# Kernel optimization log

Measured on AMD Instinct MI355X. Metric: run time of the kernel, lower is better.

The kernel has to match this reference:

```python
import jax, jax.numpy as jnp
import numpy as np

N_NODES = 100000
N_DIH = 1000000
SCALAR_DIM = 128
HIDDEN = 64
ATTR_DIM = 3


def setup_inputs() -> dict:
    key = jax.random.key(0)
    ks = jax.random.split(key, 10)
    x = jax.random.normal(ks[0], (N_NODES, SCALAR_DIM), dtype=jnp.float32)
    quadra_index = jax.random.randint(ks[1], (4, N_DIH), 0, N_NODES, dtype=jnp.int32)
    quadra_attr = jax.random.normal(ks[2], (N_DIH, ATTR_DIM), dtype=jnp.float32)
    d_in = SCALAR_DIM * 2 + ATTR_DIM
    W1 = jax.random.normal(ks[3], (d_in, HIDDEN), dtype=jnp.float32) / np.sqrt(d_in)
    b1 = jnp.zeros((HIDDEN,), dtype=jnp.float32)
    W2 = jax.random.normal(ks[4], (HIDDEN, HIDDEN), dtype=jnp.float32) / np.sqrt(HIDDEN)
    b2 = jnp.zeros((HIDDEN,), dtype=jnp.float32)
    W3 = jax.random.normal(ks[5], (HIDDEN, SCALAR_DIM), dtype=jnp.float32) / np.sqrt(HIDDEN)
    b3 = jnp.zeros((SCALAR_DIM,), dtype=jnp.float32)
    # o3.Linear on pure scalars ('128x0e'->'128x0e') is a bias-free linear map
    Wout = jax.random.normal(ks[6], (SCALAR_DIM, SCALAR_DIM), dtype=jnp.float32) / np.sqrt(SCALAR_DIM)
    return {"x": x, "quadra_index": quadra_index, "quadra_attr": quadra_attr,
            "W1": W1, "b1": b1, "W2": W2, "b2": b2, "W3": W3, "b3": b3, "Wout": Wout}


def _scatter_mean(msgs, idx, num_segments):
    sums = jax.ops.segment_sum(msgs, idx, num_segments=num_segments)
    counts = jax.ops.segment_sum(jnp.ones((msgs.shape[0],), msgs.dtype), idx,
                                 num_segments=num_segments)
    return sums / jnp.maximum(counts, 1.0)[:, None]


def reference(x, quadra_index, quadra_attr, W1, b1, W2, b2, W3, b3, Wout):
    n = x.shape[0]
    x_scalar = x[:, :SCALAR_DIM]
    i, j, k, l = quadra_index[0], quadra_index[1], quadra_index[2], quadra_index[3]
    # gather endpoints, concat with dihedral attrs: [E, 2*D + 3]
    dih_in = jnp.concatenate([x_scalar[i], x_scalar[l], quadra_attr], axis=-1)
    h = jax.nn.silu(dih_in @ W1 + b1)
    h = jax.nn.silu(h @ W2 + b2)
    msgs = h @ W3 + b3  # [E, D]
    aggr_j = _scatter_mean(msgs, j, n)
    aggr_k = _scatter_mean(msgs, k, n)
    aggr = (aggr_j + aggr_k) * 0.5
    return aggr @ Wout
```

## Files before the change

kernel.cpp:

```cpp
#include <hip/hip_runtime.h>

#define N_NODES    100000
#define N_DIH      1000000
#define SCALAR_DIM 128
#define HIDDEN     64
#define ATTR_DIM   3

typedef short v8s __attribute__((ext_vector_type(8)));
typedef float v4f __attribute__((ext_vector_type(4)));

__device__ __forceinline__ float silu(float v) {
    return __fdividef(v, 1.0f + __expf(-v));
}

__device__ __forceinline__ unsigned short bf16_rne(float f) {
    unsigned int u = __float_as_uint(f);
    u = (u + 0x7FFFu + ((u >> 16) & 1u)) >> 16;
    return (unsigned short)u;
}

__device__ __forceinline__ float2 bf2_to_f2(unsigned int v) {
    float2 r;
    r.x = __uint_as_float(v << 16);
    r.y = __uint_as_float(v & 0xffff0000u);
    return r;
}

#define PREP_W   112
#define PREP_W34 33
#define PREP_G   64
#define PREP_H   3907
#define PREP_XB  12500
#define PREP_MAIN (PREP_W + PREP_W34 + PREP_G + PREP_H)
#define PREP_ALL  (PREP_MAIN + PREP_XB)

__global__ void prep_kernel(const float* __restrict__ x, unsigned short* __restrict__ xb,
                            const float* __restrict__ W1, const float* __restrict__ W2,
                            const float* __restrict__ W3, const float* __restrict__ b1,
                            const float* __restrict__ b3,
                            const float* __restrict__ Wout,
                            unsigned short* __restrict__ W1f, unsigned short* __restrict__ W2f,
                            unsigned short* __restrict__ W3f, unsigned short* __restrict__ W1g,
                            float* __restrict__ W34, float* __restrict__ b34,
                            float* __restrict__ PK,
                            const int* __restrict__ qidx,
                            int* __restrict__ cnt_j, int* __restrict__ cnt_k,
                            int* __restrict__ rank_j, int* __restrict__ rank_k) {
    const int b = blockIdx.x;
    if (b < PREP_W) {
        const int tid = b * 256 + threadIdx.x;
        if (tid < 16384) {
            const int j = tid & 7, lane = (tid >> 3) & 63, t = tid >> 9;
            const int k = (t >> 2) * 32 + ((lane >> 4) << 3) + j;
            const int n = (t & 3) * 16 + (lane & 15);
            W1f[tid] = bf16_rne(W1[k * 64 + n]);
        } else if (tid < 20480) {
            const int i = tid - 16384;
            const int j = i & 7, lane = (i >> 3) & 63, t = i >> 9;
            const int k = (t >> 2) * 32 + ((lane >> 4) << 3) + j;
            const int n = (t & 3) * 16 + (lane & 15);
            W2f[i] = bf16_rne(W2[k * 64 + n]);
        } else if (tid < 28672) {
            const int i = tid - 20480;
            const int j = i & 7, lane = (i >> 3) & 63, t = i >> 9;
            const int k = (t >> 3) * 32 + ((lane >> 4) << 3) + j;
            const int n = (t & 7) * 16 + (lane & 15);
            W3f[i] = bf16_rne(W3[k * 128 + n]);
        }
    } else if (b < PREP_W + PREP_W34) {
        const int t34 = (b - PREP_W) * 256 + threadIdx.x;
        if (t34 < 8192) {
            const int r = t34 >> 7, c = t34 & 127;
            float s = 0.f;
            #pragma unroll 4
            for (int m = 0; m < 128; ++m) s += W3[r * 128 + m] * Wout[m * 128 + c];
            W34[t34] = s;
        } else if (t34 < 8320) {
            const int c = t34 - 8192;
            float s = 0.f;
            #pragma unroll 4
            for (int m = 0; m < 128; ++m) s += b3[m] * Wout[m * 128 + c];
            b34[c] = s;
        } else if (t34 < 8384) {
            const int c = t34 - 8320;
            PK[c * 4 + 0] = W1[256 * 64 + c];
            PK[c * 4 + 1] = W1[257 * 64 + c];
            PK[c * 4 + 2] = W1[258 * 64 + c];
            PK[c * 4 + 3] = b1[c];
        }
    } else if (b < PREP_W + PREP_W34 + PREP_G) {
        const int i = (b - PREP_W - PREP_W34) * 256 + threadIdx.x;
        const int j = i & 7, lane = (i >> 3) & 63, t = i >> 9;
        const int k = (t >> 3) * 32 + ((lane >> 4) << 3) + j;
        const int n = (t & 7) * 16 + (lane & 15);
        const float w = (n < 64) ? W1[k * 64 + n] : W1[(128 + k) * 64 + (n - 64)];
        W1g[i] = bf16_rne(w);
    } else if (b < PREP_MAIN) {
        const int t = (b - PREP_W - PREP_W34 - PREP_G) * 256 + threadIdx.x;
        if (t < N_DIH) {
            const int rj = atomicAdd(&cnt_j[qidx[N_DIH + t]], 1);
            const int rk = atomicAdd(&cnt_k[qidx[2 * N_DIH + t]], 1);
            if (rank_j != nullptr) {
                rank_j[t] = rj;
                rank_k[t] = rk;
            }
        }
    } else {
        const int t = (b - PREP_MAIN) * 256 + threadIdx.x;
        const float4 v = *(const float4*)&x[(size_t)t * 4];
        ushort4 o;
        o.x = bf16_rne(v.x); o.y = bf16_rne(v.y); o.z = bf16_rne(v.z); o.w = bf16_rne(v.w);
        *(ushort4*)&xb[(size_t)t * 4] = o;
    }
}

__global__ __launch_bounds__(1024) void scan_kernel(const int* __restrict__ cnt_j,
                                                    const int* __restrict__ cnt_k,
                                                    int* __restrict__ off_j, int* __restrict__ off_k) {
    const int* cnt = blockIdx.x ? cnt_k : cnt_j;
    int* off = blockIdx.x ? off_k : off_j;
    __shared__ int wtot[17];
    const int tid = threadIdx.x, lane = tid & 63, wv = tid >> 6;
    int carry = 0;
    for (int base = 0; base < N_NODES; base += 1024) {
        const int i = base + tid;
        const int v = (i < N_NODES) ? cnt[i] : 0;
        int inc = v;
        #pragma unroll
        for (int o = 1; o < 64; o <<= 1) {
            const int t = __shfl_up(inc, o);
            if (lane >= o) inc += t;
        }
        if (lane == 63) wtot[wv] = inc;
        __syncthreads();
        if (tid == 0) {
            int run = 0;
            #pragma unroll
            for (int w = 0; w < 16; ++w) { const int t = wtot[w]; wtot[w] = run; run += t; }
            wtot[16] = run;
        }
        __syncthreads();
        const int excl = inc - v + wtot[wv] + carry;
        if (i < N_NODES) off[i] = excl;
        carry += wtot[16];
        __syncthreads();
    }
    if (tid == 0) off[N_NODES] = carry;
}

__global__ void permute_kernel(const int* __restrict__ qidx,
                               const int* __restrict__ off_j, const int* __restrict__ off_k,
                               const int* __restrict__ rank_j, const int* __restrict__ rank_k,
                               int* __restrict__ perm_j, int* __restrict__ perm_k) {
    const int t = blockIdx.x * blockDim.x + threadIdx.x;
    if (t < N_DIH) {
        const int j = qidx[N_DIH + t];
        perm_j[off_j[j] + rank_j[t]] = t;
        const int k = qidx[2 * N_DIH + t];
        perm_k[off_k[k] + rank_k[t]] = t;
    }
}

#define UVW 3125

__global__ __launch_bounds__(256, 4) void uv_kernel(
    const float* __restrict__ x, const unsigned short* __restrict__ W1g,
    float* __restrict__ uv)
{
    const int tid = threadIdx.x, lane = tid & 63, wv = tid >> 6;
    const int g = blockIdx.x * 4 + wv;
    if (g >= UVW) return;
    const int D0 = g * 32;
    const int m16 = lane & 15, quad = lane >> 4;
    const int r0 = D0 + m16, r1 = D0 + 16 + m16;

    v4f acc[2][8];
    #pragma unroll
    for (int mt = 0; mt < 2; ++mt)
        #pragma unroll
        for (int nt = 0; nt < 8; ++nt) acc[mt][nt] = (v4f){0.f, 0.f, 0.f, 0.f};

    #pragma unroll
    for (int kc = 0; kc < 4; ++kc) {
        const int co = kc * 32 + quad * 8;
        v8s a0, a1;
        {
            const float4 f0 = *(const float4*)&x[(size_t)r0 * 128 + co];
            const float4 f1 = *(const float4*)&x[(size_t)r0 * 128 + co + 4];
            a0[0] = (short)bf16_rne(f0.x); a0[1] = (short)bf16_rne(f0.y);
            a0[2] = (short)bf16_rne(f0.z); a0[3] = (short)bf16_rne(f0.w);
            a0[4] = (short)bf16_rne(f1.x); a0[5] = (short)bf16_rne(f1.y);
            a0[6] = (short)bf16_rne(f1.z); a0[7] = (short)bf16_rne(f1.w);
        }
        {
            const float4 f0 = *(const float4*)&x[(size_t)r1 * 128 + co];
            const float4 f1 = *(const float4*)&x[(size_t)r1 * 128 + co + 4];
            a1[0] = (short)bf16_rne(f0.x); a1[1] = (short)bf16_rne(f0.y);
            a1[2] = (short)bf16_rne(f0.z); a1[3] = (short)bf16_rne(f0.w);
            a1[4] = (short)bf16_rne(f1.x); a1[5] = (short)bf16_rne(f1.y);
            a1[6] = (short)bf16_rne(f1.z); a1[7] = (short)bf16_rne(f1.w);
        }
        #pragma unroll
        for (int nt = 0; nt < 8; ++nt) {
            const v8s bf = *(const v8s*)(W1g + ((kc * 8 + nt) * 64 + lane) * 8);
            acc[0][nt] = __builtin_amdgcn_mfma_f32_16x16x32_bf16(a0, bf, acc[0][nt], 0, 0, 0);
            acc[1][nt] = __builtin_amdgcn_mfma_f32_16x16x32_bf16(a1, bf, acc[1][nt], 0, 0, 0);
        }
    }
    #pragma unroll
    for (int mt = 0; mt < 2; ++mt)
        #pragma unroll
        for (int nt = 0; nt < 8; ++nt) {
            const int c = nt * 16 + m16;
            #pragma unroll
            for (int reg = 0; reg < 4; ++reg) {
                const int n = D0 + mt * 16 + quad * 4 + reg;
                uv[(size_t)n * 128 + c] = acc[mt][nt][reg];
            }
        }
}

#define NW16 62500

__global__ __launch_bounds__(256, 6) void mlp2_kernel(
    const float* __restrict__ uv, const int* __restrict__ qidx,
    const float* __restrict__ attr, const float* __restrict__ PK,
    const unsigned short* __restrict__ W2f, const float* __restrict__ b2,
    unsigned short* __restrict__ h2)
{
    __shared__ __align__(16) unsigned short hbuf[4][1024];
    const int tid = threadIdx.x, lane = tid & 63, wv = tid >> 6;
    const int g = blockIdx.x * 4 + wv;
    const int D0 = g * 16;
    const int m16 = lane & 15, quad = lane >> 4;
    unsigned short* hs = hbuf[wv];

    const int d = D0 + m16;
    const int irow = qidx[d];
    const int lrow = qidx[3 * N_DIH + d];

    const float* up = uv + (size_t)irow * 128 + quad * 8;
    const float* vp = uv + (size_t)lrow * 128 + 64 + quad * 8;
    const float4 u00 = *(const float4*)(up + 0);
    const float4 u01 = *(const float4*)(up + 4);
    const float4 u10 = *(const float4*)(up + 32);
    const float4 u11 = *(const float4*)(up + 36);
    const float4 v00 = *(const float4*)(vp + 0);
    const float4 v01 = *(const float4*)(vp + 4);
    const float4 v10 = *(const float4*)(vp + 32);
    const float4 v11 = *(const float4*)(vp + 36);
    const float a0 = attr[(size_t)d * 3 + 0];
    const float a1 = attr[(size_t)d * 3 + 1];
    const float a2 = attr[(size_t)d * 3 + 2];

    const int cb = quad * 8;
    v8s af0, af1;
#define EL(dst, e, cc, uval, vval) { \
    const float4 pk = *(const float4*)&PK[(size_t)(cc) * 4]; \
    const float s = (uval) + (vval) + pk.x * a0 + pk.y * a1 + pk.z * a2 + pk.w; \
    dst[e] = (short)bf16_rne(silu(s)); }
    EL(af0, 0, cb + 0,      u00.x, v00.x)
    EL(af0, 1, cb + 1,      u00.y, v00.y)
    EL(af0, 2, cb + 2,      u00.z, v00.z)
    EL(af0, 3, cb + 3,      u00.w, v00.w)
    EL(af0, 4, cb + 4,      u01.x, v01.x)
    EL(af0, 5, cb + 5,      u01.y, v01.y)
    EL(af0, 6, cb + 6,      u01.z, v01.z)
    EL(af0, 7, cb + 7,      u01.w, v01.w)
    EL(af1, 0, 32 + cb + 0, u10.x, v10.x)
    EL(af1, 1, 32 + cb + 1, u10.y, v10.y)
    EL(af1, 2, 32 + cb + 2, u10.z, v10.z)
    EL(af1, 3, 32 + cb + 3, u10.w, v10.w)
    EL(af1, 4, 32 + cb + 4, u11.x, v11.x)
    EL(af1, 5, 32 + cb + 5, u11.y, v11.y)
    EL(af1, 6, 32 + cb + 6, u11.z, v11.z)
    EL(af1, 7, 32 + cb + 7, u11.w, v11.w)
#undef EL

    v4f acc2[4];
    #pragma unroll
    for (int nt = 0; nt < 4; ++nt) acc2[nt] = (v4f){0.f, 0.f, 0.f, 0.f};
    #pragma unroll
    for (int nt = 0; nt < 4; ++nt) {
        const v8s bA = *(const v8s*)(W2f + ((nt) * 64 + lane) * 8);
        const v8s bB = *(const v8s*)(W2f + ((4 + nt) * 64 + lane) * 8);
        acc2[nt] = __builtin_amdgcn_mfma_f32_16x16x32_bf16(af0, bA, acc2[nt], 0, 0, 0);
        acc2[nt] = __builtin_amdgcn_mfma_f32_16x16x32_bf16(af1, bB, acc2[nt], 0, 0, 0);
    }

    #pragma unroll
    for (int nt = 0; nt < 4; ++nt) {
        const int c = nt * 16 + m16;
        const float b2c = b2[c];
        #pragma unroll
        for (int reg = 0; reg < 4; ++reg) {
            const int row = quad * 4 + reg;
            hs[row * 64 + c] = bf16_rne(silu(acc2[nt][reg] + b2c));
        }
    }
    #pragma unroll
    for (int i = 0; i < 2; ++i) {
        const v8s row16 = *(const v8s*)(hs + i * 512 + lane * 8);
        *(v8s*)(h2 + (size_t)D0 * 64 + i * 512 + lane * 8) = row16;
    }
}

#define NWAVES 31250

__global__ __launch_bounds__(256, 8) void mlp12_kernel(
    const unsigned short* __restrict__ xb, const int* __restrict__ qidx,
    const float* __restrict__ attr,
    const float* __restrict__ W1, const float* __restrict__ b1,
    const float* __restrict__ b2,
    const unsigned short* __restrict__ W1f, const unsigned short* __restrict__ W2f,
    unsigned short* __restrict__ h2)
{
    __shared__ __align__(16) unsigned short hbuf[4][1024];
    const int tid  = threadIdx.x;
    const int lane = tid & 63;
    const int wv   = tid >> 6;
    const int g    = blockIdx.x * 4 + wv;
    const int D0   = g * 16;
    const int m16  = lane & 15;
    const int quad = lane >> 4;
    unsigned short* hs = hbuf[wv];

    const int irow = qidx[D0 + m16];
    const int lrow = qidx[3 * N_DIH + D0 + m16];

    v4f acc[4];
    #pragma unroll
    for (int nt = 0; nt < 4; ++nt) acc[nt] = (v4f){0.f, 0.f, 0.f, 0.f};

    #pragma unroll
    for (int kc = 0; kc < 8; ++kc) {
        const int side = kc >> 2;
        const int coff = (kc & 3) * 32 + quad * 8;
        const int r0 = side ? lrow : irow;
        const v8s a0 = *(const v8s*)(xb + (size_t)r0 * 128 + coff);
        #pragma unroll
        for (int nt = 0; nt < 4; ++nt) {
            const v8s b = *(const v8s*)(W1f + ((kc * 4 + nt) * 64 + lane) * 8);
            acc[nt] = __builtin_amdgcn_mfma_f32_16x16x32_bf16(a0, b, acc[nt], 0, 0, 0);
        }
    }

    #pragma unroll
    for (int nt = 0; nt < 4; ++nt) {
        const int c = nt * 16 + m16;
        const float b1c = b1[c];
        const float wa0 = W1[256 * 64 + c];
        const float wa1 = W1[257 * 64 + c];
        const float wa2 = W1[258 * 64 + c];
        const int quadp = (nt * 2 + (m16 >> 3)) & 3;
        const int jp    = m16 & 7;
        const int kc2   = nt >> 1;
        #pragma unroll
        for (int reg = 0; reg < 4; ++reg) {
            const int r = quad * 4 + reg;
            const int d = D0 + r;
            float v = acc[nt][reg] + b1c
                    + attr[(size_t)d * 3 + 0] * wa0
                    + attr[(size_t)d * 3 + 1] * wa1
                    + attr[(size_t)d * 3 + 2] * wa2;
            v = silu(v);
            hs[kc2 * 512 + (r + 16 * quadp) * 8 + jp] = bf16_rne(v);
        }
    }

    v4f acc2[4];
    #pragma unroll
    for (int nt = 0; nt < 4; ++nt) acc2[nt] = (v4f){0.f, 0.f, 0.f, 0.f};

    #pragma unroll
    for (int kc = 0; kc < 2; ++kc) {
        const v8s a0 = *(const v8s*)(hs + kc * 512 + lane * 8);
        #pragma unroll
        for (int nt = 0; nt < 4; ++nt) {
            const v8s b = *(const v8s*)(W2f + ((kc * 4 + nt) * 64 + lane) * 8);
            acc2[nt] = __builtin_amdgcn_mfma_f32_16x16x32_bf16(a0, b, acc2[nt], 0, 0, 0);
        }
    }

    #pragma unroll
    for (int nt = 0; nt < 4; ++nt) {
        const int c = nt * 16 + m16;
        const float b2c = b2[c];
        #pragma unroll
        for (int reg = 0; reg < 4; ++reg) {
            const int row = quad * 4 + reg;
            hs[row * 64 + c] = bf16_rne(silu(acc2[nt][reg] + b2c));
        }
    }
    #pragma unroll
    for (int i = 0; i < 2; ++i) {
        const v8s row16 = *(const v8s*)(hs + i * 512 + lane * 8);
        *(v8s*)(h2 + (size_t)D0 * 64 + i * 512 + lane * 8) = row16;
    }
}

__global__ __launch_bounds__(256, 2) void aggregate_out64(
    const unsigned short* __restrict__ h2,
    const int* __restrict__ off_j, const int* __restrict__ off_k,
    const int* __restrict__ perm_j, const int* __restrict__ perm_k,
    const float* __restrict__ W34, const float* __restrict__ b34,
    float* __restrict__ out)
{
    __shared__ float a_lds[64 * 132];
    const int tid    = threadIdx.x;
    const int lane   = tid & 63;
    const int wv     = __builtin_amdgcn_readfirstlane(tid >> 6);
    const int base   = blockIdx.x * 64;
    const int half   = lane >> 5;
    const int lane31 = lane & 31;

    for (int p = 0; p < 16; ++p) {
        const int ln = wv * 16 + p;
        const int n  = base + ln;
        float sx = 0.f, sy = 0.f, bf = 0.f;
        if (n < N_NODES) {
            int cj, ck;
            {
                const int e0 = off_j[n], e1 = off_j[n + 1];
                cj = e1 - e0;
                float ax = 0.f, ay = 0.f;
                int e = e0;
                for (; e + 4 <= e1; e += 4) {
                    const int dA = perm_j[e + half];
                    const int dB = perm_j[e + 2 + half];
                    const float2 fA = bf2_to_f2(*(const unsigned int*)(h2 + (size_t)dA * 64 + lane31 * 2));
                    const float2 fB = bf2_to_f2(*(const unsigned int*)(h2 + (size_t)dB * 64 + lane31 * 2));
                    ax += fA.x + fB.x; ay += fA.y + fB.y;
                }
                if (e + 2 <= e1) {
                    const int d = perm_j[e + half];
                    const float2 f = bf2_to_f2(*(const unsigned int*)(h2 + (size_t)d * 64 + lane31 * 2));
                    ax += f.x; ay += f.y;
                    e += 2;
                }
                if (e < e1 && half == 0) {
                    const int d = perm_j[e];
                    const float2 f = bf2_to_f2(*(const unsigned int*)(h2 + (size_t)d * 64 + lane31 * 2));
                    ax += f.x; ay += f.y;
                }
                ax += __shfl_xor(ax, 32);
                ay += __shfl_xor(ay, 32);
                const float inv = 1.0f / (float)max(cj, 1);
                sx += ax * inv; sy += ay * inv;
            }
            {
                const int e0 = off_k[n], e1 = off_k[n + 1];
                ck = e1 - e0;
                float ax = 0.f, ay = 0.f;
                int e = e0;
                for (; e + 4 <= e1; e += 4) {
                    const int dA = perm_k[e + half];
                    const int dB = perm_k[e + 2 + half];
                    const float2 fA = bf2_to_f2(*(const unsigned int*)(h2 + (size_t)dA * 64 + lane31 * 2));
                    const float2 fB = bf2_to_f2(*(const unsigned int*)(h2 + (size_t)dB * 64 + lane31 * 2));
                    ax += fA.x + fB.x; ay += fA.y + fB.y;
                }
                if (e + 2 <= e1) {
                    const int d = perm_k[e + half];
                    const float2 f = bf2_to_f2(*(const unsigned int*)(h2 + (size_t)d * 64 + lane31 * 2));
                    ax += f.x; ay += f.y;
                    e += 2;
                }
                if (e < e1 && half == 0) {
                    const int d = perm_k[e];
                    const float2 f = bf2_to_f2(*(const unsigned int*)(h2 + (size_t)d * 64 + lane31 * 2));
                    ax += f.x; ay += f.y;
                }
                ax += __shfl_xor(ax, 32);
                ay += __shfl_xor(ay, 32);
                const float inv = 1.0f / (float)max(ck, 1);
                sx += ax * inv; sy += ay * inv;
            }
            bf = 0.5f * ((float)(cj > 0) + (float)(ck > 0));
        }
        if (half == 0) {
            float2 w; w.x = sx * 0.5f; w.y = sy * 0.5f;
            *(float2*)&a_lds[ln * 132 + 2 * lane31] = w;
            if (lane31 == 0) a_lds[ln * 132 + 128] = bf;
        }
    }
    __syncthreads();

    const int co = wv * 32;
    const float bfv = a_lds[lane * 132 + 128];
    float acc[32];
    #pragma unroll
    for (int c = 0; c < 32; ++c) acc[c] = bfv * b34[co + c];
    const float* ap = &a_lds[lane * 132];
    #pragma unroll 2
    for (int d = 0; d < 64; d += 4) {
        const float4 av = *(const float4*)&ap[d];
        const float* w0 = &W34[(d + 0) * 128 + co];
        const float* w1 = w0 + 128;
        const float* w2 = w0 + 256;
        const float* w3 = w0 + 384;
        #pragma unroll
        for (int c = 0; c < 32; ++c)
            acc[c] += av.x * w0[c] + av.y * w1[c] + av.z * w2[c] + av.w * w3[c];
    }
    __syncthreads();
    #pragma unroll
    for (int c = 0; c < 32; c += 4)
        *(float4*)&a_lds[lane * 132 + co + c] = make_float4(acc[c], acc[c+1], acc[c+2], acc[c+3]);
    __syncthreads();
    const int q4 = lane31 << 2;
    #pragma unroll
    for (int p = 0; p < 8; ++p) {
        const int ln = wv * 16 + p * 2 + half;
        const int n  = base + ln;
        if (n < N_NODES)
            *(float4*)&out[(size_t)n * 128 + q4] = *(const float4*)&a_lds[ln * 132 + q4];
    }
}

__global__ void scale_kernel(const int* __restrict__ cnt_j, const int* __restrict__ cnt_k,
                             float* __restrict__ scale_j, float* __restrict__ scale_k) {
    int n = blockIdx.x * blockDim.x + threadIdx.x;
    if (n < N_NODES) {
        scale_j[n] = 0.5f / (float)max(cnt_j[n], 1);
        scale_k[n] = 0.5f / (float)max(cnt_k[n], 1);
    }
}

__global__ __launch_bounds__(256, 3) void mlp_mfma_atomic(
    const unsigned short* __restrict__ xb, const int* __restrict__ qidx,
    const float* __restrict__ attr,
    const float* __restrict__ W1, const float* __restrict__ b1,
    const float* __restrict__ b2, const float* __restrict__ b3,
    const unsigned short* __restrict__ W1f, const unsigned short* __restrict__ W2f,
    const unsigned short* __restrict__ W3f,
    const float* __restrict__ scale_j, const float* __restrict__ scale_k,
    float* __restrict__ aggr)
{
    __shared__ __align__(16) unsigned short hbuf[4][4096];
    const int tid  = threadIdx.x;
    const int lane = tid & 63;
    const int wv   = tid >> 6;
    const int g    = blockIdx.x * 4 + wv;
    if (g >= NWAVES) return;
    const int D0   = g * 32;
    const int m16  = lane & 15;
    const int quad = lane >> 4;
    unsigned short* hs = hbuf[wv];

    int irow[2], lrow[2];
    irow[0] = qidx[D0 + m16];
    irow[1] = qidx[D0 + 16 + m16];
    lrow[0] = qidx[3 * N_DIH + D0 + m16];
    lrow[1] = qidx[3 * N_DIH + D0 + 16 + m16];

    v4f acc[2][4];
    #pragma unroll
    for (int mt = 0; mt < 2; ++mt)
        #pragma unroll
        for (int nt = 0; nt < 4; ++nt) acc[mt][nt] = (v4f){0.f, 0.f, 0.f, 0.f};
    #pragma unroll
    for (int kc = 0; kc < 8; ++kc) {
        const int side = kc >> 2;
        const int coff = (kc & 3) * 32 + quad * 8;
        const int r0 = side ? lrow[0] : irow[0];
        const int r1 = side ? lrow[1] : irow[1];
        const v8s a0 = *(const v8s*)(xb + (size_t)r0 * 128 + coff);
        const v8s a1 = *(const v8s*)(xb + (size_t)r1 * 128 + coff);
        #pragma unroll
        for (int nt = 0; nt < 4; ++nt) {
            const v8s b = *(const v8s*)(W1f + ((kc * 4 + nt) * 64 + lane) * 8);
            acc[0][nt] = __builtin_amdgcn_mfma_f32_16x16x32_bf16(a0, b, acc[0][nt], 0, 0, 0);
            acc[1][nt] = __builtin_amdgcn_mfma_f32_16x16x32_bf16(a1, b, acc[1][nt], 0, 0, 0);
        }
    }
    #pragma unroll
    for (int mt = 0; mt < 2; ++mt) {
        #pragma unroll
        for (int nt = 0; nt < 4; ++nt) {
            const int c = nt * 16 + m16;
            const float b1c = b1[c];
            const float wa0 = W1[256 * 64 + c];
            const float wa1 = W1[257 * 64 + c];
            const float wa2 = W1[258 * 64 + c];
            const int quadp = (nt * 2 + (m16 >> 3)) & 3;
            const int jp    = m16 & 7;
            const int kc2   = nt >> 1;
            #pragma unroll
            for (int reg = 0; reg < 4; ++reg) {
                const int r = quad * 4 + reg;
                const int d = D0 + mt * 16 + r;
                float v = acc[mt][nt][reg] + b1c
                        + attr[(size_t)d * 3 + 0] * wa0
                        + attr[(size_t)d * 3 + 1] * wa1
                        + attr[(size_t)d * 3 + 2] * wa2;
                v = silu(v);
                hs[mt * 1024 + kc2 * 512 + (r + 16 * quadp) * 8 + jp] = bf16_rne(v);
            }
        }
    }
    v4f acc2[2][4];
    #pragma unroll
    for (int mt = 0; mt < 2; ++mt)
        #pragma unroll
        for (int nt = 0; nt < 4; ++nt) acc2[mt][nt] = (v4f){0.f, 0.f, 0.f, 0.f};
    #pragma unroll
    for (int kc = 0; kc < 2; ++kc) {
        const v8s a0 = *(const v8s*)(hs +        kc * 512 + lane * 8);
        const v8s a1 = *(const v8s*)(hs + 1024 + kc * 512 + lane * 8);
        #pragma unroll
        for (int nt = 0; nt < 4; ++nt) {
            const v8s b = *(const v8s*)(W2f + ((kc * 4 + nt) * 64 + lane) * 8);
            acc2[0][nt] = __builtin_amdgcn_mfma_f32_16x16x32_bf16(a0, b, acc2[0][nt], 0, 0, 0);
            acc2[1][nt] = __builtin_amdgcn_mfma_f32_16x16x32_bf16(a1, b, acc2[1][nt], 0, 0, 0);
        }
    }
    #pragma unroll
    for (int mt = 0; mt < 2; ++mt) {
        #pragma unroll
        for (int nt = 0; nt < 4; ++nt) {
            const float b2c = b2[nt * 16 + m16];
            const int quadp = (nt * 2 + (m16 >> 3)) & 3;
            const int jp    = m16 & 7;
            const int kc2   = nt >> 1;
            #pragma unroll
            for (int reg = 0; reg < 4; ++reg) {
                const int r = quad * 4 + reg;
                const float v = silu(acc2[mt][nt][reg] + b2c);
                hs[2048 + mt * 1024 + kc2 * 512 + (r + 16 * quadp) * 8 + jp] = bf16_rne(v);
            }
        }
    }
    v4f acc3[2][8];
    #pragma unroll
    for (int mt = 0; mt < 2; ++mt)
        #pragma unroll
        for (int nt = 0; nt < 8; ++nt) acc3[mt][nt] = (v4f){0.f, 0.f, 0.f, 0.f};
    #pragma unroll
    for (int kc = 0; kc < 2; ++kc) {
        const v8s a0 = *(const v8s*)(hs + 2048 +        kc * 512 + lane * 8);
        const v8s a1 = *(const v8s*)(hs + 2048 + 1024 + kc * 512 + lane * 8);
        #pragma unroll
        for (int nt = 0; nt < 8; ++nt) {
            const v8s b = *(const v8s*)(W3f + ((kc * 8 + nt) * 64 + lane) * 8);
            acc3[0][nt] = __builtin_amdgcn_mfma_f32_16x16x32_bf16(a0, b, acc3[0][nt], 0, 0, 0);
            acc3[1][nt] = __builtin_amdgcn_mfma_f32_16x16x32_bf16(a1, b, acc3[1][nt], 0, 0, 0);
        }
    }
    #pragma unroll
    for (int mt = 0; mt < 2; ++mt) {
        int jn[4], kn[4]; float sjv[4], skv[4];
        #pragma unroll
        for (int reg = 0; reg < 4; ++reg) {
            const int d = D0 + mt * 16 + quad * 4 + reg;
            jn[reg] = qidx[N_DIH + d];
            kn[reg] = qidx[2 * N_DIH + d];
            sjv[reg] = scale_j[jn[reg]];
            skv[reg] = scale_k[kn[reg]];
        }
        #pragma unroll
        for (int nt = 0; nt < 8; ++nt) {
            const int c = nt * 16 + m16;
            const float b3c = b3[c];
            #pragma unroll
            for (int reg = 0; reg < 4; ++reg) {
                const float v = acc3[mt][nt][reg] + b3c;
                atomicAdd(&aggr[(size_t)jn[reg] * 128 + c], v * sjv[reg]);
                atomicAdd(&aggr[(size_t)kn[reg] * 128 + c], v * skv[reg]);
            }
        }
    }
}

#define OB    256
#define OTILE 64
__global__ __launch_bounds__(OB, 2) void out_kernel(const float* __restrict__ aggr,
                                                    const float* __restrict__ Wout,
                                                    float* __restrict__ out) {
    __shared__ float a_lds[OTILE * 132];
    const int tid  = threadIdx.x;
    const int lane = tid & 63;
    const int wv   = __builtin_amdgcn_readfirstlane(tid >> 6);
    const int base = blockIdx.x * OTILE;
    const int half = lane >> 5;
    const int q4   = (lane & 31) << 2;
    #pragma unroll
    for (int p = 0; p < 8; ++p) {
        const int ln = wv * 16 + p * 2 + half;
        const int n  = base + ln;
        float4 v = make_float4(0.f, 0.f, 0.f, 0.f);
        if (n < N_NODES) v = *(const float4*)&aggr[(size_t)n * 128 + q4];
        *(float4*)&a_lds[ln * 132 + q4] = v;
    }
    __syncthreads();
    const int c0 = wv * 32;
    float acc[32];
    #pragma unroll
    for (int c = 0; c < 32; ++c) acc[c] = 0.0f;
    const float* ap = &a_lds[lane * 132];
    #pragma unroll 2
    for (int d = 0; d < 128; d += 4) {
        const float4 av = *(const float4*)&ap[d];
        const float* w0 = &Wout[(d + 0) * 128 + c0];
        const float* w1 = &Wout[(d + 1) * 128 + c0];
        const float* w2 = &Wout[(d + 2) * 128 + c0];
        const float* w3 = &Wout[(d + 3) * 128 + c0];
        #pragma unroll
        for (int c = 0; c < 32; ++c)
            acc[c] += av.x * w0[c] + av.y * w1[c] + av.z * w2[c] + av.w * w3[c];
    }
    __syncthreads();
    #pragma unroll
    for (int c = 0; c < 32; c += 4)
        *(float4*)&a_lds[lane * 132 + c0 + c] = make_float4(acc[c], acc[c+1], acc[c+2], acc[c+3]);
    __syncthreads();
    #pragma unroll
    for (int p = 0; p < 8; ++p) {
        const int ln = wv * 16 + p * 2 + half;
        const int n  = base + ln;
        if (n < N_NODES)
            *(float4*)&out[(size_t)n * 128 + q4] = *(const float4*)&a_lds[ln * 132 + q4];
    }
}

extern "C" void kernel_launch(void* const* d_in, const int* in_sizes, int n_in,
                              void* d_out, int out_size, void* d_ws, size_t ws_size,
                              hipStream_t stream) {
    const float* x    = (const float*)d_in[0];
    const int*   qidx = (const int*)d_in[1];
    const float* attr = (const float*)d_in[2];
    const float* W1   = (const float*)d_in[3];
    const float* b1   = (const float*)d_in[4];
    const float* W2   = (const float*)d_in[5];
    const float* b2   = (const float*)d_in[6];
    const float* W3   = (const float*)d_in[7];
    const float* b3   = (const float*)d_in[8];
    const float* Wout = (const float*)d_in[9];
    float* out = (float*)d_out;
    float* wsf = (float*)d_ws;

    const size_t words = ws_size / 4;
    if (words >= (size_t)47500000) {
        size_t o = 0;
        unsigned short* h2  = (unsigned short*)wsf;          o += 32000000;
        float* uvp  = wsf + o;                               o += 12800000;
        unsigned short* W1f = (unsigned short*)(wsf + o);    o += 8192;
        unsigned short* W2f = (unsigned short*)(wsf + o);    o += 2048;
        unsigned short* W3f = (unsigned short*)(wsf + o);    o += 4096;
        unsigned short* W1g = (unsigned short*)(wsf + o);    o += 8192;
        float* W34  = wsf + o;                               o += 8192;
        float* b34  = wsf + o;                               o += 128;
        float* PK   = wsf + o;                               o += 256;
        int* cnt_j  = (int*)(wsf + o);                       o += 100000;
        int* cnt_k  = (int*)(wsf + o);                       o += 100000;
        int* off_j  = (int*)(wsf + o);                       o += 100001;
        int* off_k  = (int*)(wsf + o);                       o += 100001;
        int* perm_j = (int*)(wsf + o);                       o += 1000000;
        int* perm_k = (int*)(wsf + o);                       o += 1000000;
        int* rank_j = (int*)h2;
        int* rank_k = rank_j + N_DIH;

        hipMemsetAsync(cnt_j, 0, (size_t)200000 * sizeof(int), stream);
        prep_kernel<<<PREP_MAIN, 256, 0, stream>>>(
            x, h2 , W1, W2, W3, b1, b3, Wout,
            W1f, W2f, W3f, W1g, W34, b34, PK, qidx, cnt_j, cnt_k, rank_j, rank_k);
        scan_kernel<<<2, 1024, 0, stream>>>(cnt_j, cnt_k, off_j, off_k);
        permute_kernel<<<(N_DIH + 255) / 256, 256, 0, stream>>>(
            qidx, off_j, off_k, rank_j, rank_k, perm_j, perm_k);
        uv_kernel<<<(UVW + 3) / 4, 256, 0, stream>>>(x, W1g, uvp);
        mlp2_kernel<<<NW16 / 4, 256, 0, stream>>>(uvp, qidx, attr, PK, W2f, b2, h2);
        aggregate_out64<<<(N_NODES + 63) / 64, 256, 0, stream>>>(
            h2, off_j, off_k, perm_j, perm_k, W34, b34, out);
    } else if (words >= (size_t)41100000) {
        size_t o = 0;
        unsigned short* h2  = (unsigned short*)wsf;          o += 32000000;
        unsigned short* xb  = (unsigned short*)(wsf + o);    o += 6400000;
        unsigned short* W1f = (unsigned short*)(wsf + o);    o += 8192;
        unsigned short* W2f = (unsigned short*)(wsf + o);    o += 2048;
        unsigned short* W3f = (unsigned short*)(wsf + o);    o += 4096;
        float* W34  = wsf + o;                               o += 8192;
        float* b34  = wsf + o;                               o += 128;
        int* cnt_j  = (int*)(wsf + o);                       o += 100000;
        int* cnt_k  = (int*)(wsf + o);                       o += 100000;
        int* off_j  = (int*)(wsf + o);                       o += 100001;
        int* off_k  = (int*)(wsf + o);                       o += 100001;
        int* perm_j = (int*)(wsf + o);                       o += 1000000;
        int* perm_k = (int*)(wsf + o);                       o += 1000000;
        unsigned short* W1g = (unsigned short*)(wsf + o);    o += 8192;
        float* PK   = wsf + o;                               o += 256;
        int* rank_j = (int*)h2;
        int* rank_k = rank_j + N_DIH;

        hipMemsetAsync(cnt_j, 0, (size_t)200000 * sizeof(int), stream);
        prep_kernel<<<PREP_ALL, 256, 0, stream>>>(
            x, xb, W1, W2, W3, b1, b3, Wout,
            W1f, W2f, W3f, W1g, W34, b34, PK, qidx, cnt_j, cnt_k, rank_j, rank_k);
        scan_kernel<<<2, 1024, 0, stream>>>(cnt_j, cnt_k, off_j, off_k);
        permute_kernel<<<(N_DIH + 255) / 256, 256, 0, stream>>>(
            qidx, off_j, off_k, rank_j, rank_k, perm_j, perm_k);
        mlp12_kernel<<<NW16 / 4, 256, 0, stream>>>(
            xb, qidx, attr, W1, b1, b2, W1f, W2f, h2);
        aggregate_out64<<<(N_NODES + 63) / 64, 256, 0, stream>>>(
            h2, off_j, off_k, perm_j, perm_k, W34, b34, out);
    } else {
        int*   cnt_j   = (int*)wsf;
        int*   cnt_k   = cnt_j + N_NODES;
        float* scale_j = wsf + 200000;
        float* scale_k = wsf + 300000;
        float* aggr    = wsf + 400000;
        unsigned short* xb  = (unsigned short*)(wsf + 13200000);
        unsigned short* W1f = (unsigned short*)(wsf + 19600000);
        unsigned short* W2f = (unsigned short*)(wsf + 19608192);
        unsigned short* W3f = (unsigned short*)(wsf + 19610240);
        float* W34 = wsf + 19612288;
        float* b34 = wsf + 19612288;
        unsigned short* W1g = (unsigned short*)(wsf + 19612288);
        float* PK  = wsf + 19612288;

        hipMemsetAsync(cnt_j, 0, (size_t)2 * N_NODES * sizeof(int), stream);
        hipMemsetAsync(aggr, 0, (size_t)N_NODES * 128 * sizeof(float), stream);
        prep_kernel<<<PREP_ALL, 256, 0, stream>>>(
            x, xb, W1, W2, W3, b1, b3, Wout,
            W1f, W2f, W3f, W1g, W34, b34, PK, qidx, cnt_j, cnt_k, nullptr, nullptr);
        scale_kernel<<<(N_NODES + 255) / 256, 256, 0, stream>>>(cnt_j, cnt_k, scale_j, scale_k);
        mlp_mfma_atomic<<<(NWAVES + 3) / 4, 256, 0, stream>>>(
            xb, qidx, attr, W1, b1, b2, b3, W1f, W2f, W3f, scale_j, scale_k, aggr);
        out_kernel<<<(N_NODES + OTILE - 1) / OTILE, OB, 0, stream>>>(aggr, Wout, out);
    }
}
```

Baseline: 610.5 us.

## Scatter MLP outputs into per-node sorted buffers for sequential aggregation

Adds a new path, used when the workspace is large enough, in which the second MLP stage writes each dihedral's hidden row twice: once into a buffer sorted by j-node and once into a buffer sorted by k-node, at positions given by CSR offsets plus per-edge ranks. The aggregation kernel then reads contiguous row ranges per node instead of gathering through permutation indices. This turns random reads in aggregation into streaming reads, at the cost of doubling the hidden-state writes (scattered) and the workspace size.

```diff
diff --git a/kernel.cpp b/kernel.cpp
--- a/kernel.cpp
+++ b/kernel.cpp
@@ -222,6 +222,100 @@
 
 #define NW16 62500
 
+__global__ __launch_bounds__(256, 6) void mlp2s_kernel(
+    const float* __restrict__ uv, const int* __restrict__ qidx,
+    const float* __restrict__ attr, const float* __restrict__ PK,
+    const unsigned short* __restrict__ W2f, const float* __restrict__ b2,
+    const int* __restrict__ off_j, const int* __restrict__ off_k,
+    const int* __restrict__ rank_j, const int* __restrict__ rank_k,
+    unsigned short* __restrict__ h2j, unsigned short* __restrict__ h2k)
+{
+    __shared__ __align__(16) unsigned short hbuf[4][1024];
+    const int tid = threadIdx.x, lane = tid & 63, wv = tid >> 6;
+    const int g = blockIdx.x * 4 + wv;
+    const int D0 = g * 16;
+    const int m16 = lane & 15, quad = lane >> 4;
+    unsigned short* hs = hbuf[wv];
+
+    const int d = D0 + m16;
+    const int irow = qidx[d];
+    const int lrow = qidx[3 * N_DIH + d];
+    const int jn = qidx[N_DIH + d];
+    const int kn = qidx[2 * N_DIH + d];
+    const int pj = off_j[jn] + rank_j[d];
+    const int pk = off_k[kn] + rank_k[d];
+
+    const float* up = uv + (size_t)irow * 128 + quad * 8;
+    const float* vp = uv + (size_t)lrow * 128 + 64 + quad * 8;
+    const float4 u00 = *(const float4*)(up + 0);
+    const float4 u01 = *(const float4*)(up + 4);
+    const float4 u10 = *(const float4*)(up + 32);
+    const float4 u11 = *(const float4*)(up + 36);
+    const float4 v00 = *(const float4*)(vp + 0);
+    const float4 v01 = *(const float4*)(vp + 4);
+    const float4 v10 = *(const float4*)(vp + 32);
+    const float4 v11 = *(const float4*)(vp + 36);
+    const float a0 = attr[(size_t)d * 3 + 0];
+    const float a1 = attr[(size_t)d * 3 + 1];
+    const float a2 = attr[(size_t)d * 3 + 2];
+
+    const int cb = quad * 8;
+    v8s af0, af1;
+#define EL(dst, e, cc, uval, vval) { \
+    const float4 pkv = *(const float4*)&PK[(size_t)(cc) * 4]; \
+    const float s = (uval) + (vval) + pkv.x * a0 + pkv.y * a1 + pkv.z * a2 + pkv.w; \
+    dst[e] = (short)bf16_rne(silu(s)); }
+    EL(af0, 0, cb + 0,      u00.x, v00.x)
+    EL(af0, 1, cb + 1,      u00.y, v00.y)
+    EL(af0, 2, cb + 2,      u00.z, v00.z)
+    EL(af0, 3, cb + 3,      u00.w, v00.w)
+    EL(af0, 4, cb + 4,      u01.x, v01.x)
+    EL(af0, 5, cb + 5,      u01.y, v01.y)
+    EL(af0, 6, cb + 6,      u01.z, v01.z)
+    EL(af0, 7, cb + 7,      u01.w, v01.w)
+    EL(af1, 0, 32 + cb + 0, u10.x, v10.x)
+    EL(af1, 1, 32 + cb + 1, u10.y, v10.y)
+    EL(af1, 2, 32 + cb + 2, u10.z, v10.z)
+    EL(af1, 3, 32 + cb + 3, u10.w, v10.w)
+    EL(af1, 4, 32 + cb + 4, u11.x, v11.x)
+    EL(af1, 5, 32 + cb + 5, u11.y, v11.y)
+    EL(af1, 6, 32 + cb + 6, u11.z, v11.z)
+    EL(af1, 7, 32 + cb + 7, u11.w, v11.w)
+#undef EL
+
+    v4f acc2[4];
+    #pragma unroll
+    for (int nt = 0; nt < 4; ++nt) acc2[nt] = (v4f){0.f, 0.f, 0.f, 0.f};
+    #pragma unroll
+    for (int nt = 0; nt < 4; ++nt) {
+        const v8s bA = *(const v8s*)(W2f + ((nt) * 64 + lane) * 8);
+        const v8s bB = *(const v8s*)(W2f + ((4 + nt) * 64 + lane) * 8);
+        acc2[nt] = __builtin_amdgcn_mfma_f32_16x16x32_bf16(af0, bA, acc2[nt], 0, 0, 0);
+        acc2[nt] = __builtin_amdgcn_mfma_f32_16x16x32_bf16(af1, bB, acc2[nt], 0, 0, 0);
+    }
+
+    #pragma unroll
+    for (int nt = 0; nt < 4; ++nt) {
+        const int c = nt * 16 + m16;
+        const float b2c = b2[c];
+        #pragma unroll
+        for (int reg = 0; reg < 4; ++reg) {
+            const int row = quad * 4 + reg;
+            hs[row * 64 + c] = bf16_rne(silu(acc2[nt][reg] + b2c));
+        }
+    }
+    const int sub = lane & 7;
+    #pragma unroll
+    for (int i = 0; i < 2; ++i) {
+        const int row = i * 8 + (lane >> 3);
+        const int pjr = __shfl(pj, row);
+        const int pkr = __shfl(pk, row);
+        const v8s rowv = *(const v8s*)(hs + i * 512 + lane * 8);
+        *(v8s*)(h2j + (size_t)pjr * 64 + sub * 8) = rowv;
+        *(v8s*)(h2k + (size_t)pkr * 64 + sub * 8) = rowv;
+    }
+}
+
 __global__ __launch_bounds__(256, 6) void mlp2_kernel(
     const float* __restrict__ uv, const int* __restrict__ qidx,
     const float* __restrict__ attr, const float* __restrict__ PK,
@@ -399,6 +493,116 @@
     }
 }
 
+__global__ __launch_bounds__(256, 2) void aggregate_seq(
+    const unsigned short* __restrict__ h2j, const unsigned short* __restrict__ h2k,
+    const int* __restrict__ off_j, const int* __restrict__ off_k,
+    const float* __restrict__ W34, const float* __restrict__ b34,
+    float* __restrict__ out)
+{
+    __shared__ float a_lds[64 * 132];
+    const int tid    = threadIdx.x;
+    const int lane   = tid & 63;
+    const int wv     = __builtin_amdgcn_readfirstlane(tid >> 6);
+    const int base   = blockIdx.x * 64;
+    const int half   = lane >> 5;
+    const int lane31 = lane & 31;
+
+    for (int p = 0; p < 16; ++p) {
+        const int ln = wv * 16 + p;
+        const int n  = base + ln;
+        float sx = 0.f, sy = 0.f, bf = 0.f;
+        if (n < N_NODES) {
+            int cj, ck;
+            {
+                const int e0 = off_j[n], e1 = off_j[n + 1];
+                cj = e1 - e0;
+                float ax = 0.f, ay = 0.f;
+                int e = e0;
+                for (; e + 4 <= e1; e += 4) {
+                    const float2 fA = bf2_to_f2(*(const unsigned int*)(h2j + (size_t)(e + half) * 64 + lane31 * 2));
+                    const float2 fB = bf2_to_f2(*(const unsigned int*)(h2j + (size_t)(e + 2 + half) * 64 + lane31 * 2));
+                    ax += fA.x + fB.x; ay += fA.y + fB.y;
+                }
+                if (e + 2 <= e1) {
+                    const float2 f = bf2_to_f2(*(const unsigned int*)(h2j + (size_t)(e + half) * 64 + lane31 * 2));
+                    ax += f.x; ay += f.y;
+                    e += 2;
+                }
+                if (e < e1 && half == 0) {
+                    const float2 f = bf2_to_f2(*(const unsigned int*)(h2j + (size_t)e * 64 + lane31 * 2));
+                    ax += f.x; ay += f.y;
+                }
+                ax += __shfl_xor(ax, 32);
+                ay += __shfl_xor(ay, 32);
+                const float inv = 1.0f / (float)max(cj, 1);
+                sx += ax * inv; sy += ay * inv;
+            }
+            {
+                const int e0 = off_k[n], e1 = off_k[n + 1];
+                ck = e1 - e0;
+                float ax = 0.f, ay = 0.f;
+                int e = e0;
+                for (; e + 4 <= e1; e += 4) {
+                    const float2 fA = bf2_to_f2(*(const unsigned int*)(h2k + (size_t)(e + half) * 64 + lane31 * 2));
+                    const float2 fB = bf2_to_f2(*(const unsigned int*)(h2k + (size_t)(e + 2 + half) * 64 + lane31 * 2));
+                    ax += fA.x + fB.x; ay += fA.y + fB.y;
+                }
+                if (e + 2 <= e1) {
+                    const float2 f = bf2_to_f2(*(const unsigned int*)(h2k + (size_t)(e + half) * 64 + lane31 * 2));
+                    ax += f.x; ay += f.y;
+                    e += 2;
+                }
+                if (e < e1 && half == 0) {
+                    const float2 f = bf2_to_f2(*(const unsigned int*)(h2k + (size_t)e * 64 + lane31 * 2));
+                    ax += f.x; ay += f.y;
+                }
+                ax += __shfl_xor(ax, 32);
+                ay += __shfl_xor(ay, 32);
+                const float inv = 1.0f / (float)max(ck, 1);
+                sx += ax * inv; sy += ay * inv;
+            }
+            bf = 0.5f * ((float)(cj > 0) + (float)(ck > 0));
+        }
+        if (half == 0) {
+            float2 w; w.x = sx * 0.5f; w.y = sy * 0.5f;
+            *(float2*)&a_lds[ln * 132 + 2 * lane31] = w;
+            if (lane31 == 0) a_lds[ln * 132 + 128] = bf;
+        }
+    }
+    __syncthreads();
+
+    const int co = wv * 32;
+    const float bfv = a_lds[lane * 132 + 128];
+    float acc[32];
+    #pragma unroll
+    for (int c = 0; c < 32; ++c) acc[c] = bfv * b34[co + c];
+    const float* ap = &a_lds[lane * 132];
+    #pragma unroll 2
+    for (int d = 0; d < 64; d += 4) {
+        const float4 av = *(const float4*)&ap[d];
+        const float* w0 = &W34[(d + 0) * 128 + co];
+        const float* w1 = w0 + 128;
+        const float* w2 = w0 + 256;
+        const float* w3 = w0 + 384;
+        #pragma unroll
+        for (int c = 0; c < 32; ++c)
+            acc[c] += av.x * w0[c] + av.y * w1[c] + av.z * w2[c] + av.w * w3[c];
+    }
+    __syncthreads();
+    #pragma unroll
+    for (int c = 0; c < 32; c += 4)
+        *(float4*)&a_lds[lane * 132 + co + c] = make_float4(acc[c], acc[c+1], acc[c+2], acc[c+3]);
+    __syncthreads();
+    const int q4 = lane31 << 2;
+    #pragma unroll
+    for (int p = 0; p < 8; ++p) {
+        const int ln = wv * 16 + p * 2 + half;
+        const int n  = base + ln;
+        if (n < N_NODES)
+            *(float4*)&out[(size_t)n * 128 + q4] = *(const float4*)&a_lds[ln * 132 + q4];
+    }
+}
+
 __global__ __launch_bounds__(256, 2) void aggregate_out64(
     const unsigned short* __restrict__ h2,
     const int* __restrict__ off_j, const int* __restrict__ off_k,
@@ -740,7 +944,36 @@
     float* wsf = (float*)d_ws;
 
     const size_t words = ws_size / 4;
-    if (words >= (size_t)47500000) {
+    if (words >= (size_t)79300000) {
+        size_t o = 0;
+        unsigned short* h2j = (unsigned short*)wsf;          o += 32000000;
+        unsigned short* h2k = (unsigned short*)(wsf + o);    o += 32000000;
+        float* uvp  = wsf + o;                               o += 12800000;
+        unsigned short* W1f = (unsigned short*)(wsf + o);    o += 8192;
+        unsigned short* W2f = (unsigned short*)(wsf + o);    o += 2048;
+        unsigned short* W3f = (unsigned short*)(wsf + o);    o += 4096;
+        unsigned short* W1g = (unsigned short*)(wsf + o);    o += 8192;
+        float* W34  = wsf + o;                               o += 8192;
+        float* b34  = wsf + o;                               o += 128;
+        float* PK   = wsf + o;                               o += 256;
+        int* cnt_j  = (int*)(wsf + o);                       o += 100000;
+        int* cnt_k  = (int*)(wsf + o);                       o += 100000;
+        int* off_j  = (int*)(wsf + o);                       o += 100001;
+        int* off_k  = (int*)(wsf + o);                       o += 100001;
+        int* rank_j = (int*)(wsf + o);                       o += 1000000;
+        int* rank_k = (int*)(wsf + o);                       o += 1000000;
+
+        hipMemsetAsync(cnt_j, 0, (size_t)200000 * sizeof(int), stream);
+        prep_kernel<<<PREP_MAIN, 256, 0, stream>>>(
+            x, h2j , W1, W2, W3, b1, b3, Wout,
+            W1f, W2f, W3f, W1g, W34, b34, PK, qidx, cnt_j, cnt_k, rank_j, rank_k);
+        scan_kernel<<<2, 1024, 0, stream>>>(cnt_j, cnt_k, off_j, off_k);
+        uv_kernel<<<(UVW + 3) / 4, 256, 0, stream>>>(x, W1g, uvp);
+        mlp2s_kernel<<<NW16 / 4, 256, 0, stream>>>(
+            uvp, qidx, attr, PK, W2f, b2, off_j, off_k, rank_j, rank_k, h2j, h2k);
+        aggregate_seq<<<(N_NODES + 63) / 64, 256, 0, stream>>>(
+            h2j, h2k, off_j, off_k, W34, b34, out);
+    } else if (words >= (size_t)47500000) {
         size_t o = 0;
         unsigned short* h2  = (unsigned short*)wsf;          o += 32000000;
         float* uvp  = wsf + o;                               o += 12800000;
```

New measurement: 610.7 us. Within noise of the previous version (+0.0%).
